# Optimization experiments

Measured on AMD Instinct MI355X. Metric: run time of the kernel, lower is better.

The kernel has to match this reference:

```python
import jax, jax.numpy as jnp
import numpy as np

B = 4096
FEATURES = 4608 + 4608 + 8 + 1  # 9225
LSTM = 512
R = FEATURES / LSTM
D1 = int(FEATURES / R ** (1.0 / 3.0))
D2 = int(FEATURES / R ** (2.0 / 3.0))
ACTION_SHAPES = (64, 64, 64, 64, 64, 64, 64, 64)


def setup_inputs() -> dict:
    key = jax.random.key(0)
    ks = jax.random.split(key, 32)
    s = 0.02
    inp = {
        "actualCanvasFeatures": jax.random.normal(ks[0], (B, 4608), jnp.float32),
        "objectiveCanvasFeatures": jax.random.normal(ks[1], (B, 4608), jnp.float32),
        "last_action": jax.random.uniform(ks[2], (B, 8), jnp.float32),
        "episode_percentage": 0,
        # encoder MLP
        "W1": jax.random.normal(ks[3], (FEATURES, D1), jnp.float32) * s,
        "b1": jnp.zeros((D1,), jnp.float32),
        "W2": jax.random.normal(ks[4], (D1, D2), jnp.float32) * s,
        "b2": jnp.zeros((D2,), jnp.float32),
        "W3": jax.random.normal(ks[5], (D2, LSTM), jnp.float32) * s,
        "b3": jnp.zeros((LSTM,), jnp.float32),
        # LSTM (torch gate order i,f,g,o)
        "Wih": jax.random.normal(ks[6], (4 * LSTM, LSTM), jnp.float32) * s,
        "Whh": jax.random.normal(ks[7], (4 * LSTM, LSTM), jnp.float32) * s,
        "bih": jnp.zeros((4 * LSTM,), jnp.float32),
        "bhh": jnp.zeros((4 * LSTM,), jnp.float32),
        "h0": jnp.zeros((B, LSTM), jnp.float32),
        "c0": jnp.zeros((B, LSTM), jnp.float32),
        # decoder
        "dW1": jax.random.normal(ks[8], (LSTM, LSTM // 2), jnp.float32) * s,
        "db1": jnp.zeros((LSTM // 2,), jnp.float32),
        "headWs": tuple(jax.random.normal(ks[9 + i], (LSTM // 2, a), jnp.float32) * s
                        for i, a in enumerate(ACTION_SHAPES)),
        "headbs": tuple(jnp.zeros((a,), jnp.float32) for a in ACTION_SHAPES),
        "dWo": jax.random.normal(ks[20], (LSTM + 1, LSTM), jnp.float32) * s,
        "dbo": jnp.zeros((LSTM,), jnp.float32),
    }
    return inp


def reference(actualCanvasFeatures, objectiveCanvasFeatures, last_action,
              episode_percentage, W1, b1, W2, b2, W3, b3, Wih, Whh, bih, bhh,
              h0, c0, dW1, db1, headWs, headbs, dWo, dbo):
    b = actualCanvasFeatures.shape[0]
    ep = jnp.full((b, 1), episode_percentage, dtype=jnp.float32)
    feats = jnp.concatenate(
        [actualCanvasFeatures, objectiveCanvasFeatures, last_action, ep], axis=1)
    # encoder MLP (dropout is eval-mode identity)
    x = jax.nn.relu(feats @ W1 + b1)
    x = jax.nn.relu(x @ W2 + b2)
    x = jax.nn.relu(x @ W3 + b3)
    # single-step LSTM cell, torch gate order i,f,g,o
    gates = x @ Wih.T + bih + h0 @ Whh.T + bhh
    i, f, g, o = jnp.split(gates, 4, axis=1)
    c = jax.nn.sigmoid(f) * c0 + jax.nn.sigmoid(i) * jnp.tanh(g)
    z = jax.nn.sigmoid(o) * jnp.tanh(c)  # seed
    key = jax.random.key(42)
    actions = []
    log_probabilities = jnp.zeros((b,), jnp.float32)
    entropy = jnp.float32(0.0)
    for Wk, bk in zip(headWs, headbs):
        z1 = jax.nn.relu(z @ dW1 + db1)
        logits = z1 @ Wk + bk
        logp = jax.nn.log_softmax(logits, axis=1)
        probs = jnp.exp(logp)
        key, sk = jax.random.split(key)
        act = jax.random.categorical(sk, logits, axis=1)  # [b] int
        actions.append(act.astype(jnp.float32))
        entropy = entropy + jnp.sum(-jnp.sum(probs * logp, axis=1))
        log_probabilities = log_probabilities + jnp.take_along_axis(
            logp, act[:, None], axis=1)[:, 0]
        z = jax.nn.relu(
            jnp.concatenate([z, act.astype(jnp.float32)[:, None]], axis=1) @ dWo + dbo)
    action = jnp.stack(actions, axis=1)  # [b, n_sub_actions]
    return action, entropy, log_probabilities
```

## Files before the change

### kernel.cpp

```cpp
#include <hip/hip_runtime.h>
#include <cstdint>
#include <cstring>

typedef _Float16 f16;
typedef _Float16 f16x8 __attribute__((ext_vector_type(8)));
typedef float f32x4 __attribute__((ext_vector_type(4)));

static constexpr int kPartitionable = 1;

struct Ptr8 { const float* p[8]; };

__device__ __host__ __forceinline__ int swz(int r, int k) {
  return k ^ ((r & 7) << 3);
}

__device__ __forceinline__ void gload16(const void* g, void* l) {
  __builtin_amdgcn_global_load_lds(
      (const __attribute__((address_space(1))) unsigned int*)g,
      (__attribute__((address_space(3))) unsigned int*)l, 16, 0, 0);
}

__host__ __device__ inline void tf2x32(uint32_t k0, uint32_t k1,
                                       uint32_t x0, uint32_t x1,
                                       uint32_t& o0, uint32_t& o1) {
  uint32_t ks[3] = {k0, k1, k0 ^ k1 ^ 0x1BD11BDAu};
  uint32_t v0 = x0 + ks[0], v1 = x1 + ks[1];
  const int r0[4] = {13, 15, 26, 6};
  const int r1[4] = {17, 29, 16, 24};
  for (int g = 0; g < 5; ++g) {
    const int* rr = (g & 1) ? r1 : r0;
    for (int j = 0; j < 4; ++j) {
      v0 += v1;
      v1 = (v1 << rr[j]) | (v1 >> (32 - rr[j]));
      v1 ^= v0;
    }
    v0 += ks[(g + 1) % 3];
    v1 += ks[(g + 2) % 3] + (uint32_t)(g + 1);
  }
  o0 = v0; o1 = v1;
}

template <int BM, int BN>
__global__ __launch_bounds__(256, 2) void gemm_split(
    const f16* __restrict__ Ah, const f16* __restrict__ Al, int lda,
    const f16* __restrict__ Bh, const f16* __restrict__ Bl, int ldb,
    int K,
    const float* __restrict__ bias1, const float* __restrict__ bias2,
    int nReal, int relu, int writeF32,
    float* __restrict__ outF, f16* __restrict__ outH, f16* __restrict__ outL,
    int ldo) {
  constexpr int BK = 64;
  constexpr int TM = BM / 32;
  constexpr int TN = BN / 32;
  static_assert(BM == BN, "square tiles only");
  __shared__ f16 sAh[BM * BK];
  __shared__ f16 sAl[BM * BK];
  __shared__ f16 sBh[BN * BK];
  __shared__ f16 sBl[BN * BK];

  const int tid = threadIdx.x;
  const int wave = tid >> 6;
  const int lane = tid & 63;
  const int wm = wave & 1, wn = wave >> 1;
  const int m0 = blockIdx.x * BM;
  const int n0 = blockIdx.y * BN;

  f32x4 acc[TM][TN];
  const f32x4 zero = {0.f, 0.f, 0.f, 0.f};
#pragma unroll
  for (int i = 0; i < TM; ++i)
#pragma unroll
    for (int j = 0; j < TN; ++j) acc[i][j] = zero;

  const f16* src;
  f16* dst;
  int ld, base;
  if (wave == 0)      { src = Ah; dst = sAh; ld = lda; base = m0; }
  else if (wave == 1) { src = Al; dst = sAl; ld = lda; base = m0; }
  else if (wave == 2) { src = Bh; dst = sBh; ld = ldb; base = n0; }
  else                { src = Bl; dst = sBl; ld = ldb; base = n0; }
  constexpr int NITER = BM / 8;
  const f16* gbase = src + (size_t)(base + (lane >> 3)) * ld + (lane & 7) * 8;

  const int fr = lane & 15;
  const int q8 = (lane >> 4) * 8;
  const int sw = (fr & 7) << 3;

  for (int k0 = 0; k0 < K; k0 += BK) {
    __syncthreads();
#pragma unroll
    for (int j = 0; j < NITER; ++j)
      gload16(gbase + (size_t)(j * 8) * ld + k0, dst + j * 512);
    __syncthreads();
#pragma unroll
    for (int kk = 0; kk < BK; kk += 32) {
      const int kf = (kk + q8) ^ sw;
      f16x8 aH[TM], aL[TM], bH[TN], bL[TN];
#pragma unroll
      for (int i = 0; i < TM; ++i) {
        int off = (wm * (BM / 2) + i * 16 + fr) * BK + kf;
        aH[i] = *(const f16x8*)&sAh[off];
        aL[i] = *(const f16x8*)&sAl[off];
      }
#pragma unroll
      for (int j = 0; j < TN; ++j) {
        int off = (wn * (BN / 2) + j * 16 + fr) * BK + kf;
        bH[j] = *(const f16x8*)&sBh[off];
        bL[j] = *(const f16x8*)&sBl[off];
      }
#pragma unroll
      for (int i = 0; i < TM; ++i)
#pragma unroll
        for (int j = 0; j < TN; ++j) {
          acc[i][j] = __builtin_amdgcn_mfma_f32_16x16x32_f16(aH[i], bH[j], acc[i][j], 0, 0, 0);
          acc[i][j] = __builtin_amdgcn_mfma_f32_16x16x32_f16(aH[i], bL[j], acc[i][j], 0, 0, 0);
          acc[i][j] = __builtin_amdgcn_mfma_f32_16x16x32_f16(aL[i], bH[j], acc[i][j], 0, 0, 0);
        }
    }
  }
  const int rq = lane >> 4, cl = lane & 15;
#pragma unroll
  for (int i = 0; i < TM; ++i)
#pragma unroll
    for (int j = 0; j < TN; ++j)
#pragma unroll
      for (int r = 0; r < 4; ++r) {
        int row = m0 + wm * (BM / 2) + i * 16 + rq * 4 + r;
        int col = n0 + wn * (BN / 2) + j * 16 + cl;
        float v = acc[i][j][r];
        if (col < nReal) {
          if (bias1) v += bias1[col];
          if (bias2) v += bias2[col];
          if (relu) v = fmaxf(v, 0.f);
        } else {
          v = 0.f;
        }
        if (writeF32) {
          outF[(size_t)row * ldo + col] = v;
        } else {
          size_t o = (size_t)row * ldo + swz(row, col);
          f16 h = (f16)v;
          outH[o] = h;
          outL[o] = (f16)(v - (float)h);
        }
      }
}

__global__ void conv_feats(const float* __restrict__ A, const float* __restrict__ O,
                           const float* __restrict__ LA, const int* __restrict__ EP,
                           f16* __restrict__ H, f16* __restrict__ L) {
  uint32_t idx = blockIdx.x * 256u + threadIdx.x;
  const uint32_t total = 4096u * 9280u;
  if (idx >= total) return;
  uint32_t b = idx / 9280u, c = idx - b * 9280u;
  float v;
  if (c < 4608u) v = A[(size_t)b * 4608 + c];
  else if (c < 9216u) v = O[(size_t)b * 4608 + (c - 4608u)];
  else if (c < 9224u) v = LA[(size_t)b * 8 + (c - 9216u)];
  else if (c == 9224u) v = (float)EP[0];
  else v = 0.f;
  size_t o = (size_t)b * 9280 + swz((int)b, (int)c);
  f16 h = (f16)v;
  H[o] = h;
  L[o] = (f16)(v - (float)h);
}

__global__ void convT_kernel(const float* __restrict__ W, int Kreal, int Nreal,
                             f16* __restrict__ BtH, f16* __restrict__ BtL, int Kpad) {
  __shared__ float tile[32][33];
  int k0 = blockIdx.x * 32, n0 = blockIdx.y * 32;
  int tx = threadIdx.x, ty = threadIdx.y;
  for (int r = 0; r < 32; r += 8) {
    int k = k0 + ty + r, n = n0 + tx;
    float v = (k < Kreal && n < Nreal) ? W[(size_t)k * Nreal + n] : 0.f;
    tile[ty + r][tx] = v;
  }
  __syncthreads();
  for (int r = 0; r < 32; r += 8) {
    int n = n0 + ty + r, k = k0 + tx;
    float v = tile[tx][ty + r];
    size_t o = (size_t)n * Kpad + swz(n, k);
    f16 h = (f16)v;
    BtH[o] = h;
    BtL[o] = (f16)(v - (float)h);
  }
}

__global__ void convT_heads(Ptr8 ws, f16* __restrict__ BtH, f16* __restrict__ BtL) {
  __shared__ float tile[32][33];
  int h = blockIdx.z;
  const float* W = ws.p[h];
  int k0 = blockIdx.x * 32, n0 = blockIdx.y * 32;
  int tx = threadIdx.x, ty = threadIdx.y;
  for (int r = 0; r < 32; r += 8) {
    int k = k0 + ty + r, n = n0 + tx;
    float v = (k < 256 && n < 64) ? W[(size_t)k * 64 + n] : 0.f;
    tile[ty + r][tx] = v;
  }
  __syncthreads();
  size_t base = (size_t)h * 64 * 256;
  for (int r = 0; r < 32; r += 8) {
    int n = n0 + ty + r, k = k0 + tx;
    float v = tile[tx][ty + r];
    size_t o = base + (size_t)n * 256 + swz(n, k);
    f16 hh = (f16)v;
    BtH[o] = hh;
    BtL[o] = (f16)(v - (float)hh);
  }
}

__global__ void conv_lstmB(const float* __restrict__ Wih, const float* __restrict__ Whh,
                           f16* __restrict__ H, f16* __restrict__ L) {
  uint32_t idx = blockIdx.x * 256u + threadIdx.x;
  uint32_t n = idx >> 10, k = idx & 1023u;
  float v = (k < 512u) ? Wih[(size_t)n * 512 + k] : Whh[(size_t)n * 512 + (k - 512u)];
  size_t o = (size_t)n * 1024 + swz((int)n, (int)k);
  f16 h = (f16)v;
  H[o] = h;
  L[o] = (f16)(v - (float)h);
}

__global__ void conv_h0(const float* __restrict__ h0, f16* __restrict__ H, f16* __restrict__ L) {
  uint32_t idx = blockIdx.x * 256u + threadIdx.x;
  uint32_t b = idx >> 9, j = idx & 511u;
  float v = h0[idx];
  size_t o = (size_t)b * 1024 + swz((int)b, (int)(512 + j));
  f16 h = (f16)v;
  H[o] = h;
  L[o] = (f16)(v - (float)h);
}

__global__ void lstm_pointwise(const float* __restrict__ gates, const float* __restrict__ c0,
                               f16* __restrict__ zH, f16* __restrict__ zL) {
  uint32_t idx = blockIdx.x * 256u + threadIdx.x;
  uint32_t b = idx >> 9, n = idx & 511u;
  const float* g = gates + (size_t)b * 2048;
  float gi = g[n], gf = g[512 + n], gg = g[1024 + n], go = g[1536 + n];
  float si = 1.f / (1.f + expf(-gi));
  float sf = 1.f / (1.f + expf(-gf));
  float so = 1.f / (1.f + expf(-go));
  float c = sf * c0[idx] + si * tanhf(gg);
  float z = so * tanhf(c);
  size_t o = (size_t)b * 576 + swz((int)b, (int)n);
  f16 h = (f16)z;
  zH[o] = h;
  zL[o] = (f16)(z - (float)h);
}

__global__ void init_ws(f16* zAH, f16* zAL, f16* zBH, f16* zBL,
                        float* wsLogp, float* wsEnt) {
  uint32_t idx = blockIdx.x * 256u + threadIdx.x;
  if (idx < 4096u * 63u) {
    uint32_t b = idx / 63u, c = 513u + idx - b * 63u;
    size_t o = (size_t)b * 576 + swz((int)b, (int)c);
    zAH[o] = (f16)0.f; zAL[o] = (f16)0.f; zBH[o] = (f16)0.f; zBL[o] = (f16)0.f;
  }
  if (idx < 4096u) wsLogp[idx] = 0.f;
  if (idx == 0) *wsEnt = 0.f;
}

__device__ inline double shfl_xor_dbl(double v, int m) {
  union { double d; int i[2]; } u;
  u.d = v;
  u.i[0] = __shfl_xor(u.i[0], m);
  u.i[1] = __shfl_xor(u.i[1], m);
  return u.d;
}

__global__ void sample_head(const float* __restrict__ logits,
                            uint32_t sk0, uint32_t sk1, int head, int partitionable,
                            float* __restrict__ outAct,
                            f16* __restrict__ zH, f16* __restrict__ zL,
                            float* __restrict__ wsLogp, float* __restrict__ wsEnt) {
  int wave = threadIdx.x >> 6, lane = threadIdx.x & 63;
  int b = blockIdx.x * 4 + wave;
  float l = logits[(size_t)b * 64 + lane];

  uint32_t i = (uint32_t)b * 64u + (uint32_t)lane;
  uint32_t bits;
  if (partitionable) {
    uint32_t o0, o1;
    tf2x32(sk0, sk1, 0u, i, o0, o1);
    bits = o0 ^ o1;
  } else {
    const uint32_t H = 131072u;
    uint32_t c0, c1, o0, o1;
    int pick;
    if (i < H) { c0 = i; c1 = i + H; pick = 0; }
    else       { c0 = i - H; c1 = i; pick = 1; }
    tf2x32(sk0, sk1, c0, c1, o0, o1);
    bits = pick ? o1 : o0;
  }
  uint32_t ub = (bits >> 9) | 0x3f800000u;
  float u;
  __builtin_memcpy(&u, &ub, 4);
  u -= 1.0f;
  if (u == 0.0f) u = 1.17549435e-38f;
  double gum = -log(-log((double)u));
  double s = (double)l + gum;

  int bi = lane;
  double bv = s;
#pragma unroll
  for (int off = 1; off < 64; off <<= 1) {
    double ov = shfl_xor_dbl(bv, off);
    int oi = __shfl_xor(bi, off);
    if (ov > bv || (ov == bv && oi < bi)) { bv = ov; bi = oi; }
  }
  int act = bi;

  float m = l;
#pragma unroll
  for (int off = 1; off < 64; off <<= 1) m = fmaxf(m, __shfl_xor(m, off));
  float e = expf(l - m);
  float S = e, D = e * l;
#pragma unroll
  for (int off = 1; off < 64; off <<= 1) {
    S += __shfl_xor(S, off);
    D += __shfl_xor(D, off);
  }
  float M = m + logf(S);
  float Hrow = M - D / S;
  float l_act = __shfl(l, act);

  if (lane == 0) {
    outAct[(size_t)b * 8 + head] = (float)act;
    wsLogp[b] += (l_act - M);
    size_t zo = (size_t)b * 576 + swz(b, 512);
    zH[zo] = (f16)act;
    zL[zo] = (f16)0.f;
  }
  __shared__ float hs[4];
  if (lane == 0) hs[wave] = Hrow;
  __syncthreads();
  if (threadIdx.x == 0) atomicAdd(wsEnt, hs[0] + hs[1] + hs[2] + hs[3]);
}

__global__ void finalize_out(const float* __restrict__ wsEnt, const float* __restrict__ wsLogp,
                             float* __restrict__ out) {
  uint32_t idx = blockIdx.x * 256u + threadIdx.x;
  if (idx == 0) out[32768] = *wsEnt;
  if (idx < 4096u) out[32769 + idx] = wsLogp[idx];
}

extern "C" void kernel_launch(void* const* d_in, const int* in_sizes, int n_in,
                              void* d_out, int out_size, void* d_ws, size_t ws_size,
                              hipStream_t stream) {
  (void)in_sizes; (void)out_size; (void)ws_size;
  const float* actual = (const float*)d_in[0];
  const float* object = (const float*)d_in[1];
  const float* lastA = (const float*)d_in[2];
  const int* ep = (const int*)d_in[3];
  const float* W1 = (const float*)d_in[4];
  const float* b1 = (const float*)d_in[5];
  const float* W2 = (const float*)d_in[6];
  const float* b2 = (const float*)d_in[7];
  const float* W3 = (const float*)d_in[8];
  const float* b3 = (const float*)d_in[9];
  const float* Wih = (const float*)d_in[10];
  const float* Whh = (const float*)d_in[11];
  const float* bih = (const float*)d_in[12];
  const float* bhh = (const float*)d_in[13];
  const float* h0 = (const float*)d_in[14];
  const float* c0 = (const float*)d_in[15];
  const float* dW1 = (const float*)d_in[16];
  const float* db1 = (const float*)d_in[17];
  const float* headW[8];
  const float* headb[8];
  const float *dWo, *dbo;
  if (n_in >= 36) {
    for (int h = 0; h < 8; ++h) headW[h] = (const float*)d_in[18 + h];
    for (int h = 0; h < 8; ++h) headb[h] = (const float*)d_in[26 + h];
    dWo = (const float*)d_in[34];
    dbo = (const float*)d_in[35];
  } else {
    const float* hw = (const float*)d_in[18];
    const float* hbp = (const float*)d_in[19];
    for (int h = 0; h < 8; ++h) { headW[h] = hw + (size_t)h * 256 * 64; headb[h] = hbp + (size_t)h * 64; }
    dWo = (const float*)d_in[20];
    dbo = (const float*)d_in[21];
  }

  constexpr int Bq = 4096;
  constexpr int K1 = 9280, N1 = 3584, N1r = 3518;
  constexpr int K2 = 3584, N2 = 1408, N2r = 1342;
  constexpr int K3 = 1408, N3 = 512;
  constexpr int KL = 1024, NL = 2048;
  constexpr int KD1 = 512, ND1 = 256;
  constexpr int KH = 256;
  constexpr int KDO = 576, NDO = 512;

  uint8_t* w = (uint8_t*)d_ws;
  size_t off = 0;
  auto alloc = [&](size_t bytes) -> void* {
    off = (off + 1023) & ~(size_t)1023;
    void* p = w + off;
    off += bytes;
    return p;
  };
  f16* A1h = (f16*)alloc((size_t)Bq * K1 * 2);
  f16* A1l = (f16*)alloc((size_t)Bq * K1 * 2);
  f16* Bt1h = (f16*)alloc((size_t)N1 * K1 * 2);
  f16* Bt1l = (f16*)alloc((size_t)N1 * K1 * 2);
  f16* x1h = (f16*)alloc((size_t)Bq * K2 * 2);
  f16* x1l = (f16*)alloc((size_t)Bq * K2 * 2);
  f16* Bt2h = (f16*)alloc((size_t)N2 * K2 * 2);
  f16* Bt2l = (f16*)alloc((size_t)N2 * K2 * 2);
  size_t poff = 0;
  auto palloc = [&](size_t bytes) -> void* {
    poff = (poff + 1023) & ~(size_t)1023;
    void* p = w + poff;
    poff += bytes;
    return p;
  };
  f16* x2h = (f16*)palloc((size_t)Bq * K3 * 2);
  f16* x2l = (f16*)palloc((size_t)Bq * K3 * 2);
  f16* Bt3h = (f16*)palloc((size_t)N3 * K3 * 2);
  f16* Bt3l = (f16*)palloc((size_t)N3 * K3 * 2);
  f16* ALh = (f16*)palloc((size_t)Bq * KL * 2);
  f16* ALl = (f16*)palloc((size_t)Bq * KL * 2);
  f16* BLh = (f16*)palloc((size_t)NL * KL * 2);
  f16* BLl = (f16*)palloc((size_t)NL * KL * 2);
  float* gates = (float*)palloc((size_t)Bq * NL * 4);
  f16* zAH = (f16*)palloc((size_t)Bq * 576 * 2);
  f16* zAL = (f16*)palloc((size_t)Bq * 576 * 2);
  f16* zBH = (f16*)palloc((size_t)Bq * 576 * 2);
  f16* zBL = (f16*)palloc((size_t)Bq * 576 * 2);
  f16* Btd1h = (f16*)palloc((size_t)ND1 * KD1 * 2);
  f16* Btd1l = (f16*)palloc((size_t)ND1 * KD1 * 2);
  f16* z1h = (f16*)palloc((size_t)Bq * ND1 * 2);
  f16* z1l = (f16*)palloc((size_t)Bq * ND1 * 2);
  f16* Bthh = (f16*)palloc((size_t)8 * 64 * KH * 2);
  f16* Bthl = (f16*)palloc((size_t)8 * 64 * KH * 2);
  float* logitsF = (float*)palloc((size_t)Bq * 64 * 4);
  f16* Btdoh = (f16*)palloc((size_t)NDO * KDO * 2);
  f16* Btdol = (f16*)palloc((size_t)NDO * KDO * 2);
  float* wsLogp = (float*)palloc((size_t)Bq * 4);
  float* wsEnt = (float*)palloc(64);

  uint32_t k0 = 0u, k1 = 42u;
  uint32_t sk[8][2];
  for (int h = 0; h < 8; ++h) {
    if (kPartitionable) {
      uint32_t a0, a1, b0v, b1v;
      tf2x32(k0, k1, 0u, 0u, a0, a1);
      tf2x32(k0, k1, 0u, 1u, b0v, b1v);
      sk[h][0] = b0v; sk[h][1] = b1v;
      k0 = a0; k1 = a1;
    } else {
      uint32_t a0, a1, b0v, b1v;
      tf2x32(k0, k1, 0u, 2u, a0, a1);
      tf2x32(k0, k1, 1u, 3u, b0v, b1v);
      sk[h][0] = a1; sk[h][1] = b1v;
      k0 = a0; k1 = b0v;
    }
  }
  Ptr8 hws;
  for (int h = 0; h < 8; ++h) hws.p[h] = headW[h];

  dim3 blk(256);
  dim3 tblk(32, 8);

  conv_feats<<<(4096u * 9280u + 255) / 256, blk, 0, stream>>>(actual, object, lastA, ep, A1h, A1l);
  convT_kernel<<<dim3(K1 / 32, N1 / 32), tblk, 0, stream>>>(W1, 9225, 3518, Bt1h, Bt1l, K1);
  convT_kernel<<<dim3(K2 / 32, N2 / 32), tblk, 0, stream>>>(W2, 3518, 1342, Bt2h, Bt2l, K2);

  gemm_split<128, 128><<<dim3(Bq / 128, N1 / 128), blk, 0, stream>>>(
      A1h, A1l, K1, Bt1h, Bt1l, K1, K1, b1, nullptr, N1r, 1, 0, nullptr, x1h, x1l, K2);

  init_ws<<<(4096u * 63u + 255) / 256, blk, 0, stream>>>(zAH, zAL, zBH, zBL, wsLogp, wsEnt);
  convT_kernel<<<dim3(K3 / 32, N3 / 32), tblk, 0, stream>>>(W3, 1342, 512, Bt3h, Bt3l, K3);
  conv_lstmB<<<(2048u * 1024u) / 256, blk, 0, stream>>>(Wih, Whh, BLh, BLl);
  conv_h0<<<(4096u * 512u) / 256, blk, 0, stream>>>(h0, ALh, ALl);
  convT_kernel<<<dim3(KD1 / 32, ND1 / 32), tblk, 0, stream>>>(dW1, 512, 256, Btd1h, Btd1l, KD1);
  convT_kernel<<<dim3(KDO / 32, NDO / 32), tblk, 0, stream>>>(dWo, 513, 512, Btdoh, Btdol, KDO);
  convT_heads<<<dim3(KH / 32, 2, 8), tblk, 0, stream>>>(hws, Bthh, Bthl);

  gemm_split<128, 128><<<dim3(Bq / 128, N2 / 128), blk, 0, stream>>>(
      x1h, x1l, K2, Bt2h, Bt2l, K2, K2, b2, nullptr, N2r, 1, 0, nullptr, x2h, x2l, K3);
  gemm_split<128, 128><<<dim3(Bq / 128, N3 / 128), blk, 0, stream>>>(
      x2h, x2l, K3, Bt3h, Bt3l, K3, K3, b3, nullptr, N3, 1, 0, nullptr, ALh, ALl, KL);
  gemm_split<128, 128><<<dim3(Bq / 128, NL / 128), blk, 0, stream>>>(
      ALh, ALl, KL, BLh, BLl, KL, KL, bih, bhh, NL, 0, 1, gates, nullptr, nullptr, NL);
  lstm_pointwise<<<(4096u * 512u) / 256, blk, 0, stream>>>(gates, c0, zAH, zAL);

  for (int h = 0; h < 8; ++h) {
    f16* curH = (h & 1) ? zBH : zAH;
    f16* curL = (h & 1) ? zBL : zAL;
    f16* nxtH = (h & 1) ? zAH : zBH;
    f16* nxtL = (h & 1) ? zAL : zBL;
    gemm_split<64, 64><<<dim3(Bq / 64, ND1 / 64), blk, 0, stream>>>(
        curH, curL, 576, Btd1h, Btd1l, KD1, KD1, db1, nullptr, ND1, 1, 0, nullptr, z1h, z1l, ND1);
    gemm_split<64, 64><<<dim3(Bq / 64, 1), blk, 0, stream>>>(
        z1h, z1l, ND1, Bthh + (size_t)h * 64 * KH, Bthl + (size_t)h * 64 * KH, KH, KH,
        headb[h], nullptr, 64, 0, 1, logitsF, nullptr, nullptr, 64);
    sample_head<<<Bq / 4, blk, 0, stream>>>(logitsF, sk[h][0], sk[h][1], h, kPartitionable,
                                            (float*)d_out, curH, curL, wsLogp, wsEnt);
    gemm_split<64, 64><<<dim3(Bq / 64, NDO / 64), blk, 0, stream>>>(
        curH, curL, 576, Btdoh, Btdol, KDO, KDO, dbo, nullptr, NDO, 1, 0, nullptr, nxtH, nxtL, 576);
  }
  finalize_out<<<(4097 + 255) / 256, blk, 0, stream>>>(wsEnt, wsLogp, (float*)d_out);
}
```

Baseline: 1.874 ms.

## Fuse autoregressive decoder into one persistent kernel with fragment-major weights

Replaces the 8-iteration decoder loop, which launched four kernels per head (two small GEMMs, sampling and the dWo GEMM), with a single fused kernel. In the fused kernel each block keeps 32 rows of z, z1 and the logits in LDS, and reads weights pre-packed into MFMA fragment-major layout straight from global memory. This removes about 33 launches and the global round-trips of intermediate activations. The trade-off is only 128 blocks at one block per CU, so much of the GPU may sit idle. The input feature conversion is also vectorized to 8 elements per thread, and the entropy and log-prob accumulators now write directly into the output.

```diff
diff --git a/kernel.cpp b/kernel.cpp
--- a/kernel.cpp
+++ b/kernel.cpp
@@ -9,6 +9,7 @@
 static constexpr int kPartitionable = 1;
 
 struct Ptr8 { const float* p[8]; };
+struct Keys8 { uint32_t k[8][2]; };
 
 __device__ __host__ __forceinline__ int swz(int r, int k) {
   return k ^ ((r & 7) << 3);
@@ -150,19 +151,41 @@
                            const float* __restrict__ LA, const int* __restrict__ EP,
                            f16* __restrict__ H, f16* __restrict__ L) {
   uint32_t idx = blockIdx.x * 256u + threadIdx.x;
-  const uint32_t total = 4096u * 9280u;
-  if (idx >= total) return;
-  uint32_t b = idx / 9280u, c = idx - b * 9280u;
-  float v;
-  if (c < 4608u) v = A[(size_t)b * 4608 + c];
-  else if (c < 9216u) v = O[(size_t)b * 4608 + (c - 4608u)];
-  else if (c < 9224u) v = LA[(size_t)b * 8 + (c - 9216u)];
-  else if (c == 9224u) v = (float)EP[0];
-  else v = 0.f;
-  size_t o = (size_t)b * 9280 + swz((int)b, (int)c);
-  f16 h = (f16)v;
-  H[o] = h;
-  L[o] = (f16)(v - (float)h);
+  if (idx >= 4096u * 1160u) return;
+  uint32_t b = idx / 1160u;
+  uint32_t c = (idx - b * 1160u) * 8u;
+  float v[8];
+  if (c < 4608u) {
+    const float4* p = (const float4*)(A + (size_t)b * 4608 + c);
+    float4 x = p[0], y = p[1];
+    v[0] = x.x; v[1] = x.y; v[2] = x.z; v[3] = x.w;
+    v[4] = y.x; v[5] = y.y; v[6] = y.z; v[7] = y.w;
+  } else if (c < 9216u) {
+    const float4* p = (const float4*)(O + (size_t)b * 4608 + (c - 4608u));
+    float4 x = p[0], y = p[1];
+    v[0] = x.x; v[1] = x.y; v[2] = x.z; v[3] = x.w;
+    v[4] = y.x; v[5] = y.y; v[6] = y.z; v[7] = y.w;
+  } else if (c == 9216u) {
+#pragma unroll
+    for (int j = 0; j < 8; ++j) v[j] = LA[(size_t)b * 8 + j];
+  } else if (c == 9224u) {
+    v[0] = (float)EP[0];
+#pragma unroll
+    for (int j = 1; j < 8; ++j) v[j] = 0.f;
+  } else {
+#pragma unroll
+    for (int j = 0; j < 8; ++j) v[j] = 0.f;
+  }
+  size_t o = (size_t)b * 9280 + ((int)c ^ (((int)b & 7) << 3));
+  f16x8 hv, lv;
+#pragma unroll
+  for (int j = 0; j < 8; ++j) {
+    f16 h = (f16)v[j];
+    hv[j] = h;
+    lv[j] = (f16)(v[j] - (float)h);
+  }
+  *(f16x8*)&H[o] = hv;
+  *(f16x8*)&L[o] = lv;
 }
 
 __global__ void convT_kernel(const float* __restrict__ W, int Kreal, int Nreal,
@@ -186,27 +209,49 @@
   }
 }
 
-__global__ void convT_heads(Ptr8 ws, f16* __restrict__ BtH, f16* __restrict__ BtL) {
-  __shared__ float tile[32][33];
-  int h = blockIdx.z;
+__global__ void conv_fm(const float* __restrict__ W, int Kreal, int Nreal, int NT, int KC,
+                        f16* __restrict__ FH, f16* __restrict__ FL) {
+  int idx = blockIdx.x * 256 + threadIdx.x;
+  if (idx >= NT * KC * 64) return;
+  int lane = idx & 63;
+  int t = idx >> 6;
+  int kc = t % KC, ntile = t / KC;
+  int n = ntile * 16 + (lane & 15);
+  int k0 = kc * 32 + (lane >> 4) * 8;
+  f16x8 hv, lv;
+#pragma unroll
+  for (int j = 0; j < 8; ++j) {
+    int k = k0 + j;
+    float v = (k < Kreal && n < Nreal) ? W[(size_t)k * Nreal + n] : 0.f;
+    f16 h = (f16)v;
+    hv[j] = h;
+    lv[j] = (f16)(v - (float)h);
+  }
+  *(f16x8*)&FH[(size_t)idx * 8] = hv;
+  *(f16x8*)&FL[(size_t)idx * 8] = lv;
+}
+
+__global__ void conv_fm_heads(Ptr8 ws, f16* __restrict__ FH, f16* __restrict__ FL) {
+  int h = blockIdx.y;
+  int idx = blockIdx.x * 256 + threadIdx.x;
+  if (idx >= 2048) return;
+  int lane = idx & 63;
+  int t = idx >> 6;
+  int kc = t & 7, ntile = t >> 3;
+  int n = ntile * 16 + (lane & 15);
+  int k0 = kc * 32 + (lane >> 4) * 8;
   const float* W = ws.p[h];
-  int k0 = blockIdx.x * 32, n0 = blockIdx.y * 32;
-  int tx = threadIdx.x, ty = threadIdx.y;
-  for (int r = 0; r < 32; r += 8) {
-    int k = k0 + ty + r, n = n0 + tx;
-    float v = (k < 256 && n < 64) ? W[(size_t)k * 64 + n] : 0.f;
-    tile[ty + r][tx] = v;
-  }
-  __syncthreads();
-  size_t base = (size_t)h * 64 * 256;
-  for (int r = 0; r < 32; r += 8) {
-    int n = n0 + ty + r, k = k0 + tx;
-    float v = tile[tx][ty + r];
-    size_t o = base + (size_t)n * 256 + swz(n, k);
+  f16x8 hv, lv;
+#pragma unroll
+  for (int j = 0; j < 8; ++j) {
+    float v = W[(size_t)(k0 + j) * 64 + n];
     f16 hh = (f16)v;
-    BtH[o] = hh;
-    BtL[o] = (f16)(v - (float)hh);
-  }
+    hv[j] = hh;
+    lv[j] = (f16)(v - (float)hh);
+  }
+  size_t base = (size_t)h * 16384 + (size_t)idx * 8;
+  *(f16x8*)&FH[base] = hv;
+  *(f16x8*)&FL[base] = lv;
 }
 
 __global__ void conv_lstmB(const float* __restrict__ Wih, const float* __restrict__ Whh,
@@ -247,16 +292,16 @@
   zL[o] = (f16)(z - (float)h);
 }
 
-__global__ void init_ws(f16* zAH, f16* zAL, f16* zBH, f16* zBL,
-                        float* wsLogp, float* wsEnt) {
+__global__ void init_pads(f16* __restrict__ zAH, f16* __restrict__ zAL,
+                          float* __restrict__ out) {
   uint32_t idx = blockIdx.x * 256u + threadIdx.x;
-  if (idx < 4096u * 63u) {
-    uint32_t b = idx / 63u, c = 513u + idx - b * 63u;
-    size_t o = (size_t)b * 576 + swz((int)b, (int)c);
-    zAH[o] = (f16)0.f; zAL[o] = (f16)0.f; zBH[o] = (f16)0.f; zBL[o] = (f16)0.f;
-  }
-  if (idx < 4096u) wsLogp[idx] = 0.f;
-  if (idx == 0) *wsEnt = 0.f;
+  if (idx < 4096u * 8u) {
+    uint32_t b = idx >> 3, c8 = 512u + (idx & 7u) * 8u;
+    f16x8 zz = {0, 0, 0, 0, 0, 0, 0, 0};
+    *(f16x8*)&zAH[(size_t)b * 576 + c8] = zz;
+    *(f16x8*)&zAL[(size_t)b * 576 + c8] = zz;
+  }
+  if (idx == 0) out[32768] = 0.f;
 }
 
 __device__ inline double shfl_xor_dbl(double v, int m) {
@@ -267,80 +312,221 @@
   return u.d;
 }
 
-__global__ void sample_head(const float* __restrict__ logits,
-                            uint32_t sk0, uint32_t sk1, int head, int partitionable,
-                            float* __restrict__ outAct,
-                            f16* __restrict__ zH, f16* __restrict__ zL,
-                            float* __restrict__ wsLogp, float* __restrict__ wsEnt) {
-  int wave = threadIdx.x >> 6, lane = threadIdx.x & 63;
-  int b = blockIdx.x * 4 + wave;
-  float l = logits[(size_t)b * 64 + lane];
-
-  uint32_t i = (uint32_t)b * 64u + (uint32_t)lane;
-  uint32_t bits;
-  if (partitionable) {
-    uint32_t o0, o1;
-    tf2x32(sk0, sk1, 0u, i, o0, o1);
-    bits = o0 ^ o1;
-  } else {
-    const uint32_t H = 131072u;
-    uint32_t c0, c1, o0, o1;
-    int pick;
-    if (i < H) { c0 = i; c1 = i + H; pick = 0; }
-    else       { c0 = i - H; c1 = i; pick = 1; }
-    tf2x32(sk0, sk1, c0, c1, o0, o1);
-    bits = pick ? o1 : o0;
-  }
-  uint32_t ub = (bits >> 9) | 0x3f800000u;
-  float u;
-  __builtin_memcpy(&u, &ub, 4);
-  u -= 1.0f;
-  if (u == 0.0f) u = 1.17549435e-38f;
-  double gum = -log(-log((double)u));
-  double s = (double)l + gum;
-
-  int bi = lane;
-  double bv = s;
-#pragma unroll
-  for (int off = 1; off < 64; off <<= 1) {
-    double ov = shfl_xor_dbl(bv, off);
-    int oi = __shfl_xor(bi, off);
-    if (ov > bv || (ov == bv && oi < bi)) { bv = ov; bi = oi; }
-  }
-  int act = bi;
-
-  float m = l;
-#pragma unroll
-  for (int off = 1; off < 64; off <<= 1) m = fmaxf(m, __shfl_xor(m, off));
-  float e = expf(l - m);
-  float S = e, D = e * l;
-#pragma unroll
-  for (int off = 1; off < 64; off <<= 1) {
-    S += __shfl_xor(S, off);
-    D += __shfl_xor(D, off);
-  }
-  float M = m + logf(S);
-  float Hrow = M - D / S;
-  float l_act = __shfl(l, act);
-
+__global__ __launch_bounds__(256, 1) void decoder_fused(
+    const f16* __restrict__ zH0, const f16* __restrict__ zL0,
+    const f16* __restrict__ FM1h, const f16* __restrict__ FM1l,
+    const float* __restrict__ db1,
+    const f16* __restrict__ FMhh, const f16* __restrict__ FMhl,
+    Ptr8 hb,
+    const f16* __restrict__ FMoh, const f16* __restrict__ FMol,
+    const float* __restrict__ dbo,
+    Keys8 sk, int partitionable, float* __restrict__ out) {
+  constexpr int ZS = 576, Z1S = 256;
+  __shared__ f16 zbH[32 * ZS], zbL[32 * ZS];
+  __shared__ f16 z1H[32 * Z1S], z1L[32 * Z1S];
+  __shared__ float lgt[32 * 64];
+  __shared__ float entSh[4];
+  const int tid = threadIdx.x;
+  const int wave = tid >> 6, lane = tid & 63;
+  const int fr = lane & 15, rq = lane >> 4, q8 = rq * 8;
+  const int sw = (fr & 7) << 3;
+  const int b0 = blockIdx.x * 32;
+  const f32x4 zero = {0.f, 0.f, 0.f, 0.f};
+
+  for (int t = tid; t < 2304; t += 256) {
+    ((f16x8*)zbH)[t] = ((const f16x8*)(zH0 + (size_t)b0 * ZS))[t];
+    ((f16x8*)zbL)[t] = ((const f16x8*)(zL0 + (size_t)b0 * ZS))[t];
+  }
+  float entAcc = 0.f;
+  float logpAcc[8] = {0.f, 0.f, 0.f, 0.f, 0.f, 0.f, 0.f, 0.f};
+
+  for (int h = 0; h < 8; ++h) {
+    __syncthreads();
+    {
+      f32x4 acc[2][4];
+#pragma unroll
+      for (int i = 0; i < 2; ++i)
+#pragma unroll
+        for (int j = 0; j < 4; ++j) acc[i][j] = zero;
+      for (int kc = 0; kc < 16; ++kc) {
+        int kf = (kc * 32 + q8) ^ sw;
+        f16x8 aH[2], aL[2];
+#pragma unroll
+        for (int i = 0; i < 2; ++i) {
+          int off = (i * 16 + fr) * ZS + kf;
+          aH[i] = *(const f16x8*)&zbH[off];
+          aL[i] = *(const f16x8*)&zbL[off];
+        }
+#pragma unroll
+        for (int j = 0; j < 4; ++j) {
+          size_t fo = (size_t)((wave * 4 + j) * 16 + kc) * 512 + lane * 8;
+          f16x8 bH = *(const f16x8*)&FM1h[fo];
+          f16x8 bL = *(const f16x8*)&FM1l[fo];
+#pragma unroll
+          for (int i = 0; i < 2; ++i) {
+            acc[i][j] = __builtin_amdgcn_mfma_f32_16x16x32_f16(aH[i], bH, acc[i][j], 0, 0, 0);
+            acc[i][j] = __builtin_amdgcn_mfma_f32_16x16x32_f16(aH[i], bL, acc[i][j], 0, 0, 0);
+            acc[i][j] = __builtin_amdgcn_mfma_f32_16x16x32_f16(aL[i], bH, acc[i][j], 0, 0, 0);
+          }
+        }
+      }
+#pragma unroll
+      for (int j = 0; j < 4; ++j) {
+        int col = (wave * 4 + j) * 16 + fr;
+        float bb = db1[col];
+#pragma unroll
+        for (int i = 0; i < 2; ++i)
+#pragma unroll
+          for (int r = 0; r < 4; ++r) {
+            int row = i * 16 + rq * 4 + r;
+            float v = fmaxf(acc[i][j][r] + bb, 0.f);
+            f16 hv = (f16)v;
+            int po = row * Z1S + (col ^ ((row & 7) << 3));
+            z1H[po] = hv;
+            z1L[po] = (f16)(v - (float)hv);
+          }
+      }
+    }
+    __syncthreads();
+    {
+      f32x4 acc2[2] = {zero, zero};
+      const int r0 = (wave & 1) * 16;
+      const int tb = (wave >> 1) * 2;
+      for (int kc = 0; kc < 8; ++kc) {
+        int kf = (kc * 32 + q8) ^ sw;
+        int off = (r0 + fr) * Z1S + kf;
+        f16x8 aH = *(const f16x8*)&z1H[off];
+        f16x8 aL = *(const f16x8*)&z1L[off];
+#pragma unroll
+        for (int j = 0; j < 2; ++j) {
+          size_t fo = (size_t)(h * 32 + (tb + j) * 8 + kc) * 512 + lane * 8;
+          f16x8 bH = *(const f16x8*)&FMhh[fo];
+          f16x8 bL = *(const f16x8*)&FMhl[fo];
+          acc2[j] = __builtin_amdgcn_mfma_f32_16x16x32_f16(aH, bH, acc2[j], 0, 0, 0);
+          acc2[j] = __builtin_amdgcn_mfma_f32_16x16x32_f16(aH, bL, acc2[j], 0, 0, 0);
+          acc2[j] = __builtin_amdgcn_mfma_f32_16x16x32_f16(aL, bH, acc2[j], 0, 0, 0);
+        }
+      }
+#pragma unroll
+      for (int j = 0; j < 2; ++j) {
+        int col = (tb + j) * 16 + fr;
+        float bb = hb.p[h][col];
+#pragma unroll
+        for (int r = 0; r < 4; ++r) lgt[(r0 + rq * 4 + r) * 64 + col] = acc2[j][r] + bb;
+      }
+    }
+    __syncthreads();
+    for (int rr = 0; rr < 8; ++rr) {
+      int row = wave * 8 + rr;
+      int b = b0 + row;
+      float l = lgt[row * 64 + lane];
+      uint32_t i = (uint32_t)b * 64u + (uint32_t)lane;
+      uint32_t bits;
+      if (partitionable) {
+        uint32_t o0, o1;
+        tf2x32(sk.k[h][0], sk.k[h][1], 0u, i, o0, o1);
+        bits = o0 ^ o1;
+      } else {
+        const uint32_t Hh = 131072u;
+        uint32_t c0, c1, o0, o1;
+        int pick;
+        if (i < Hh) { c0 = i; c1 = i + Hh; pick = 0; }
+        else        { c0 = i - Hh; c1 = i; pick = 1; }
+        tf2x32(sk.k[h][0], sk.k[h][1], c0, c1, o0, o1);
+        bits = pick ? o1 : o0;
+      }
+      uint32_t ub = (bits >> 9) | 0x3f800000u;
+      float u;
+      __builtin_memcpy(&u, &ub, 4);
+      u -= 1.0f;
+      if (u == 0.0f) u = 1.17549435e-38f;
+      double gum = -log(-log((double)u));
+      double s = (double)l + gum;
+      int bi = lane;
+      double bv = s;
+#pragma unroll
+      for (int off = 1; off < 64; off <<= 1) {
+        double ov = shfl_xor_dbl(bv, off);
+        int oi = __shfl_xor(bi, off);
+        if (ov > bv || (ov == bv && oi < bi)) { bv = ov; bi = oi; }
+      }
+      int act = bi;
+      float m = l;
+#pragma unroll
+      for (int off = 1; off < 64; off <<= 1) m = fmaxf(m, __shfl_xor(m, off));
+      float e = expf(l - m);
+      float S = e, D = e * l;
+#pragma unroll
+      for (int off = 1; off < 64; off <<= 1) {
+        S += __shfl_xor(S, off);
+        D += __shfl_xor(D, off);
+      }
+      float M = m + logf(S);
+      entAcc += (M - D / S);
+      float l_act = __shfl(l, act);
+      logpAcc[rr] += (l_act - M);
+      if (lane == 0) {
+        out[(size_t)b * 8 + h] = (float)act;
+        int po = row * ZS + (512 ^ ((row & 7) << 3));
+        zbH[po] = (f16)act;
+        zbL[po] = (f16)0.f;
+      }
+    }
+    __syncthreads();
+    {
+      f32x4 acc4[2][8];
+#pragma unroll
+      for (int i = 0; i < 2; ++i)
+#pragma unroll
+        for (int j = 0; j < 8; ++j) acc4[i][j] = zero;
+      for (int kc = 0; kc < 18; ++kc) {
+        int kf = (kc * 32 + q8) ^ sw;
+        f16x8 aH[2], aL[2];
+#pragma unroll
+        for (int i = 0; i < 2; ++i) {
+          int off = (i * 16 + fr) * ZS + kf;
+          aH[i] = *(const f16x8*)&zbH[off];
+          aL[i] = *(const f16x8*)&zbL[off];
+        }
+#pragma unroll
+        for (int j = 0; j < 8; ++j) {
+          size_t fo = (size_t)((wave * 8 + j) * 18 + kc) * 512 + lane * 8;
+          f16x8 bH = *(const f16x8*)&FMoh[fo];
+          f16x8 bL = *(const f16x8*)&FMol[fo];
+#pragma unroll
+          for (int i = 0; i < 2; ++i) {
+            acc4[i][j] = __builtin_amdgcn_mfma_f32_16x16x32_f16(aH[i], bH, acc4[i][j], 0, 0, 0);
+            acc4[i][j] = __builtin_amdgcn_mfma_f32_16x16x32_f16(aH[i], bL, acc4[i][j], 0, 0, 0);
+            acc4[i][j] = __builtin_amdgcn_mfma_f32_16x16x32_f16(aL[i], bH, acc4[i][j], 0, 0, 0);
+          }
+        }
+      }
+      __syncthreads();
+#pragma unroll
+      for (int j = 0; j < 8; ++j) {
+        int col = wave * 128 + j * 16 + fr;
+        float bb = dbo[col];
+#pragma unroll
+        for (int i = 0; i < 2; ++i)
+#pragma unroll
+          for (int r = 0; r < 4; ++r) {
+            int row = i * 16 + rq * 4 + r;
+            float v = fmaxf(acc4[i][j][r] + bb, 0.f);
+            f16 hv = (f16)v;
+            int po = row * ZS + (col ^ ((row & 7) << 3));
+            zbH[po] = hv;
+            zbL[po] = (f16)(v - (float)hv);
+          }
+      }
+    }
+  }
+  if (lane == 0) entSh[wave] = entAcc;
+  __syncthreads();
+  if (tid == 0) atomicAdd(&out[32768], entSh[0] + entSh[1] + entSh[2] + entSh[3]);
   if (lane == 0) {
-    outAct[(size_t)b * 8 + head] = (float)act;
-    wsLogp[b] += (l_act - M);
-    size_t zo = (size_t)b * 576 + swz(b, 512);
-    zH[zo] = (f16)act;
-    zL[zo] = (f16)0.f;
-  }
-  __shared__ float hs[4];
-  if (lane == 0) hs[wave] = Hrow;
-  __syncthreads();
-  if (threadIdx.x == 0) atomicAdd(wsEnt, hs[0] + hs[1] + hs[2] + hs[3]);
-}
-
-__global__ void finalize_out(const float* __restrict__ wsEnt, const float* __restrict__ wsLogp,
-                             float* __restrict__ out) {
-  uint32_t idx = blockIdx.x * 256u + threadIdx.x;
-  if (idx == 0) out[32768] = *wsEnt;
-  if (idx < 4096u) out[32769 + idx] = wsLogp[idx];
+#pragma unroll
+    for (int rr = 0; rr < 8; ++rr) out[32769 + b0 + wave * 8 + rr] = logpAcc[rr];
+  }
 }
 
 extern "C" void kernel_launch(void* const* d_in, const int* in_sizes, int n_in,
@@ -386,9 +572,6 @@
   constexpr int K2 = 3584, N2 = 1408, N2r = 1342;
   constexpr int K3 = 1408, N3 = 512;
   constexpr int KL = 1024, NL = 2048;
-  constexpr int KD1 = 512, ND1 = 256;
-  constexpr int KH = 256;
-  constexpr int KDO = 576, NDO = 512;
 
   uint8_t* w = (uint8_t*)d_ws;
   size_t off = 0;
@@ -424,57 +607,50 @@
   float* gates = (float*)palloc((size_t)Bq * NL * 4);
   f16* zAH = (f16*)palloc((size_t)Bq * 576 * 2);
   f16* zAL = (f16*)palloc((size_t)Bq * 576 * 2);
-  f16* zBH = (f16*)palloc((size_t)Bq * 576 * 2);
-  f16* zBL = (f16*)palloc((size_t)Bq * 576 * 2);
-  f16* Btd1h = (f16*)palloc((size_t)ND1 * KD1 * 2);
-  f16* Btd1l = (f16*)palloc((size_t)ND1 * KD1 * 2);
-  f16* z1h = (f16*)palloc((size_t)Bq * ND1 * 2);
-  f16* z1l = (f16*)palloc((size_t)Bq * ND1 * 2);
-  f16* Bthh = (f16*)palloc((size_t)8 * 64 * KH * 2);
-  f16* Bthl = (f16*)palloc((size_t)8 * 64 * KH * 2);
-  float* logitsF = (float*)palloc((size_t)Bq * 64 * 4);
-  f16* Btdoh = (f16*)palloc((size_t)NDO * KDO * 2);
-  f16* Btdol = (f16*)palloc((size_t)NDO * KDO * 2);
-  float* wsLogp = (float*)palloc((size_t)Bq * 4);
-  float* wsEnt = (float*)palloc(64);
+  f16* FM1h = (f16*)palloc((size_t)16 * 16 * 512 * 2);
+  f16* FM1l = (f16*)palloc((size_t)16 * 16 * 512 * 2);
+  f16* FMhh = (f16*)palloc((size_t)8 * 32 * 512 * 2);
+  f16* FMhl = (f16*)palloc((size_t)8 * 32 * 512 * 2);
+  f16* FMoh = (f16*)palloc((size_t)32 * 18 * 512 * 2);
+  f16* FMol = (f16*)palloc((size_t)32 * 18 * 512 * 2);
 
   uint32_t k0 = 0u, k1 = 42u;
-  uint32_t sk[8][2];
+  Keys8 sk;
   for (int h = 0; h < 8; ++h) {
     if (kPartitionable) {
       uint32_t a0, a1, b0v, b1v;
       tf2x32(k0, k1, 0u, 0u, a0, a1);
       tf2x32(k0, k1, 0u, 1u, b0v, b1v);
-      sk[h][0] = b0v; sk[h][1] = b1v;
+      sk.k[h][0] = b0v; sk.k[h][1] = b1v;
       k0 = a0; k1 = a1;
     } else {
       uint32_t a0, a1, b0v, b1v;
       tf2x32(k0, k1, 0u, 2u, a0, a1);
       tf2x32(k0, k1, 1u, 3u, b0v, b1v);
-      sk[h][0] = a1; sk[h][1] = b1v;
+      sk.k[h][0] = a1; sk.k[h][1] = b1v;
       k0 = a0; k1 = b0v;
     }
   }
-  Ptr8 hws;
-  for (int h = 0; h < 8; ++h) hws.p[h] = headW[h];
+  Ptr8 hws, hbs;
+  for (int h = 0; h < 8; ++h) { hws.p[h] = headW[h]; hbs.p[h] = headb[h]; }
 
   dim3 blk(256);
   dim3 tblk(32, 8);
 
-  conv_feats<<<(4096u * 9280u + 255) / 256, blk, 0, stream>>>(actual, object, lastA, ep, A1h, A1l);
+  conv_feats<<<(4096u * 1160u + 255) / 256, blk, 0, stream>>>(actual, object, lastA, ep, A1h, A1l);
   convT_kernel<<<dim3(K1 / 32, N1 / 32), tblk, 0, stream>>>(W1, 9225, 3518, Bt1h, Bt1l, K1);
   convT_kernel<<<dim3(K2 / 32, N2 / 32), tblk, 0, stream>>>(W2, 3518, 1342, Bt2h, Bt2l, K2);
 
   gemm_split<128, 128><<<dim3(Bq / 128, N1 / 128), blk, 0, stream>>>(
       A1h, A1l, K1, Bt1h, Bt1l, K1, K1, b1, nullptr, N1r, 1, 0, nullptr, x1h, x1l, K2);
 
-  init_ws<<<(4096u * 63u + 255) / 256, blk, 0, stream>>>(zAH, zAL, zBH, zBL, wsLogp, wsEnt);
+  init_pads<<<(4096u * 8u + 255) / 256, blk, 0, stream>>>(zAH, zAL, (float*)d_out);
   convT_kernel<<<dim3(K3 / 32, N3 / 32), tblk, 0, stream>>>(W3, 1342, 512, Bt3h, Bt3l, K3);
   conv_lstmB<<<(2048u * 1024u) / 256, blk, 0, stream>>>(Wih, Whh, BLh, BLl);
   conv_h0<<<(4096u * 512u) / 256, blk, 0, stream>>>(h0, ALh, ALl);
-  convT_kernel<<<dim3(KD1 / 32, ND1 / 32), tblk, 0, stream>>>(dW1, 512, 256, Btd1h, Btd1l, KD1);
-  convT_kernel<<<dim3(KDO / 32, NDO / 32), tblk, 0, stream>>>(dWo, 513, 512, Btdoh, Btdol, KDO);
-  convT_heads<<<dim3(KH / 32, 2, 8), tblk, 0, stream>>>(hws, Bthh, Bthl);
+  conv_fm<<<(16 * 16 * 64 + 255) / 256, blk, 0, stream>>>(dW1, 512, 256, 16, 16, FM1h, FM1l);
+  conv_fm<<<(32 * 18 * 64 + 255) / 256, blk, 0, stream>>>(dWo, 513, 512, 32, 18, FMoh, FMol);
+  conv_fm_heads<<<dim3(8, 8), blk, 0, stream>>>(hws, FMhh, FMhl);
 
   gemm_split<128, 128><<<dim3(Bq / 128, N2 / 128), blk, 0, stream>>>(
       x1h, x1l, K2, Bt2h, Bt2l, K2, K2, b2, nullptr, N2r, 1, 0, nullptr, x2h, x2l, K3);
@@ -484,20 +660,7 @@
       ALh, ALl, KL, BLh, BLl, KL, KL, bih, bhh, NL, 0, 1, gates, nullptr, nullptr, NL);
   lstm_pointwise<<<(4096u * 512u) / 256, blk, 0, stream>>>(gates, c0, zAH, zAL);
 
-  for (int h = 0; h < 8; ++h) {
-    f16* curH = (h & 1) ? zBH : zAH;
-    f16* curL = (h & 1) ? zBL : zAL;
-    f16* nxtH = (h & 1) ? zAH : zBH;
-    f16* nxtL = (h & 1) ? zAL : zBL;
-    gemm_split<64, 64><<<dim3(Bq / 64, ND1 / 64), blk, 0, stream>>>(
-        curH, curL, 576, Btd1h, Btd1l, KD1, KD1, db1, nullptr, ND1, 1, 0, nullptr, z1h, z1l, ND1);
-    gemm_split<64, 64><<<dim3(Bq / 64, 1), blk, 0, stream>>>(
-        z1h, z1l, ND1, Bthh + (size_t)h * 64 * KH, Bthl + (size_t)h * 64 * KH, KH, KH,
-        headb[h], nullptr, 64, 0, 1, logitsF, nullptr, nullptr, 64);
-    sample_head<<<Bq / 4, blk, 0, stream>>>(logitsF, sk[h][0], sk[h][1], h, kPartitionable,
-                                            (float*)d_out, curH, curL, wsLogp, wsEnt);
-    gemm_split<64, 64><<<dim3(Bq / 64, NDO / 64), blk, 0, stream>>>(
-        curH, curL, 576, Btdoh, Btdol, KDO, KDO, dbo, nullptr, NDO, 1, 0, nullptr, nxtH, nxtL, 576);
-  }
-  finalize_out<<<(4097 + 255) / 256, blk, 0, stream>>>(wsEnt, wsLogp, (float*)d_out);
-}
+  decoder_fused<<<128, blk, 0, stream>>>(
+      zAH, zAL, FM1h, FM1l, db1, FMhh, FMhl, hbs, FMoh, FMol, dbo,
+      sk, kPartitionable, (float*)d_out);
+}
```

New measurement: 1.883 ms. About the same (+0.5%).
